# Kernel tuning notes

Hardware: AMD Instinct MI355X
Metric: run time of the kernel (lower is better)

Reference implementation:

```python
import jax, jax.numpy as jnp
import numpy as np

B, N, H, F = 256, 256, 256, 64   # batch, nodes, hidden, output
NNB = 4                          # neighbors per node (nns - 1)
HEADS = 3
S = 2 ** NNB - 1                 # nonempty subsets for Mobius Choquet
# MASK[s, i] = True iff neighbor i is in subset s (subsets 1..2^n-1)
MASK = jnp.asarray(np.array([[(s >> i) & 1 for i in range(NNB)] for s in range(1, S + 1)], dtype=bool))


def setup_inputs() -> dict:
    key = jax.random.key(0)
    ks = jax.random.split(key, 12)
    w = 0.02
    centers = jnp.arange(N, dtype=jnp.int64)[:, None]
    neigh = jax.random.randint(ks[11], (N, NNB), 0, N).astype(jnp.int64)
    local_edges = jnp.concatenate([centers, neigh], axis=1)[:, None, :]  # [N, 1, 5]
    return {
        "observation": jax.random.normal(ks[0], (B, N, H), jnp.float32),
        "action": jax.random.normal(ks[1], (B, N, H), jnp.float32),
        "V_W1": jax.random.normal(ks[2], (N, H, H), jnp.float32) * w,
        "V_b1": jnp.zeros((N, H), jnp.float32),
        "V_W2": jax.random.normal(ks[3], (N, H, F), jnp.float32) * w,
        "V_b2": jnp.zeros((N, F), jnp.float32),
        "A_W1": jax.random.normal(ks[4], (N, 2 * H, H), jnp.float32) * w,
        "A_b1": jnp.zeros((N, H), jnp.float32),
        "A_W2": jax.random.normal(ks[5], (N, H, F), jnp.float32) * w,
        "A_b2": jnp.zeros((N, F), jnp.float32),
        "chi_m": jax.random.normal(ks[6], (N, HEADS, S), jnp.float32) * w,
        "local_edges": local_edges,
    }


def _mmlp2(x, W1, b1, W2, b2):
    # per-node (multi) 2-layer MLP: first layer ReLU, second linear (act=False)
    h = jax.nn.relu(jnp.einsum('bni,nio->bno', x, W1) + b1)
    return jnp.einsum('bnh,nho->bno', h, W2) + b2


def reference(observation, action, V_W1, V_b1, V_W2, V_b2,
              A_W1, A_b1, A_W2, A_b2, chi_m, local_edges):
    V = _mmlp2(observation, V_W1, V_b1, V_W2, V_b2)                      # [B,N,F]
    A = _mmlp2(jnp.concatenate([observation, action], axis=-1),
               A_W1, A_b1, A_W2, A_b2)                                   # [B,N,F]
    Q = A + V                                                            # [B,N,F]
    centers = local_edges[:, 0, 0]        # [N]
    neigh = local_edges[:, 0, 1:]         # [N, NNB]
    # .data in torch -> detach the gathered neighbor Q-values
    Qn = jax.lax.stop_gradient(Q[:, neigh, :])                           # [B,N,NNB,F]
    # Mobius Choquet: min over each nonempty subset of neighbors
    masked = jnp.where(MASK[None, None, :, :, None], Qn[:, :, None, :, :], jnp.inf)
    mins = masked.min(axis=3)                                            # [B,N,S,F]
    chi = jnp.einsum('bnsf,nhs->bnf', mins, chi_m) / HEADS               # [B,N,F]
    return (chi + Q[:, centers, :]).mean(axis=-1)                        # [B,N]
```

## Files before the change

### kernel.cpp

```cpp
#include <hip/hip_runtime.h>
#include <cstddef>


#define BN 256
#define HD 256
#define FD 64
#define NHD (BN * HD)
#define XS 40

typedef _Float16 f16x8 __attribute__((ext_vector_type(8)));
typedef _Float16 f16x4 __attribute__((ext_vector_type(4)));
typedef float f32x4 __attribute__((ext_vector_type(4)));

#define BAR_LGKM()                                                         \
  asm volatile("s_waitcnt lgkmcnt(0)" ::: "memory");                       \
  __builtin_amdgcn_s_barrier();                                            \
  asm volatile("" ::: "memory");

__device__ __forceinline__ void x_load(const float* xs0, const float* xs1, int n,
                                       int row0, int kt, int tid, float4 xr[2]) {
  int kOff = kt * 32;
  const float* xs = (kOff < 256) ? xs0 : xs1;
  int row = tid >> 2, c = (tid & 3) * 4;
  const float* p = xs + (size_t)(row0 + row) * NHD + n * HD + (kOff & 255) + c;
  xr[0] = *(const float4*)p;
  xr[1] = *(const float4*)(p + 16);
}
__device__ __forceinline__ void x_write(_Float16* Xl, int tid, const float4 xr[2]) {
  int row = tid >> 2, c = (tid & 3) * 4;
  f16x4 a, b;
  a[0] = (_Float16)xr[0].x; a[1] = (_Float16)xr[0].y;
  a[2] = (_Float16)xr[0].z; a[3] = (_Float16)xr[0].w;
  b[0] = (_Float16)xr[1].x; b[1] = (_Float16)xr[1].y;
  b[2] = (_Float16)xr[1].z; b[3] = (_Float16)xr[1].w;
  *(f16x4*)(Xl + row * XS + c) = a;
  *(f16x4*)(Xl + row * XS + c + 16) = b;
}

__device__ __forceinline__ void w1_stage(const float* __restrict__ Wg, _Float16* Wl,
                                         int kt, int w, int l) {
#pragma unroll
  for (int cg = 0; cg < 4; ++cg) {
    int col = cg * 64 + l;
    const float* p = Wg + (size_t)(kt * 32 + w * 8) * HD + col;
    f16x8 v;
#pragma unroll
    for (int r = 0; r < 8; ++r) v[r] = (_Float16)p[(size_t)r * HD];
    *(f16x8*)(Wl + ((size_t)(w * 256 + col)) * 8) = v;
  }
}

__device__ __forceinline__ void w2_stage(const float* __restrict__ W2g, _Float16* Wl,
                                         int half, int w, int l) {
#pragma unroll
  for (int cg = 0; cg < 4; ++cg) {
    int khi = w * 4 + cg;
    const float* p = W2g + (size_t)(half * 128 + khi * 8) * FD + l;
    f16x8 v;
#pragma unroll
    for (int r = 0; r < 8; ++r) v[r] = (_Float16)p[(size_t)r * FD];
    *(f16x8*)(Wl + ((size_t)(khi * 64 + l)) * 8) = v;
  }
}

__device__ __forceinline__ void g1_compute(const _Float16* Wl, const _Float16* Xl,
                                           int lrow, int lq, int Nbase,
                                           f32x4 acc[4][4]) {
  f16x8 b[4];
#pragma unroll
  for (int nf = 0; nf < 4; ++nf)
    b[nf] = *(const f16x8*)(Wl + ((size_t)(lq * 256 + Nbase + nf * 16 + lrow)) * 8);
#pragma unroll
  for (int m = 0; m < 4; ++m) {
    f16x8 a = *(const f16x8*)(Xl + (m * 16 + lrow) * XS + lq * 8);
#pragma unroll
    for (int nf = 0; nf < 4; ++nf)
      acc[m][nf] = __builtin_amdgcn_mfma_f32_16x16x32_f16(a, b[nf], acc[m][nf], 0, 0, 0);
  }
}

template <int NK>
__device__ __forceinline__ void run_gemm1(const float* xs0, const float* xs1,
                                          const float* __restrict__ Wg,
                                          int n, int row0, int tid, int lrow, int lq,
                                          int Nbase, int w, int l,
                                          _Float16* Wl, _Float16* Xl,
                                          f32x4 acc[4][4]) {
  float4 xr[2];
  x_load(xs0, xs1, n, row0, 0, tid, xr);
  w1_stage(Wg, Wl, 0, w, l);
  x_write(Xl, tid, xr);
#pragma unroll 1
  for (int kt = 0; kt < NK; ++kt) {
    BAR_LGKM();
    if (kt + 1 < NK) x_load(xs0, xs1, n, row0, kt + 1, tid, xr);
    g1_compute(Wl, Xl, lrow, lq, Nbase, acc);
    BAR_LGKM();
    if (kt + 1 < NK) {
      w1_stage(Wg, Wl, kt + 1, w, l);
      x_write(Xl, tid, xr);
    }
  }
}

__device__ __forceinline__ void gemm2_branch(const f32x4 acc[4][4], f32x4 acc2[4],
                                             const float* __restrict__ W2g,
                                             const float* __restrict__ b1g,
                                             _Float16* Wl, _Float16* slab,
                                             int lrow, int lq, int Nbase, int w, int l) {
  float bv[4];
#pragma unroll
  for (int nf = 0; nf < 4; ++nf) bv[nf] = b1g[Nbase + nf * 16 + lrow];
  w2_stage(W2g, Wl, 0, w, l);
#pragma unroll
  for (int s = 0; s < 8; ++s) {
    if (w == (s >> 1)) {
#pragma unroll
      for (int m = 0; m < 4; ++m)
#pragma unroll
        for (int nf2 = 0; nf2 < 2; ++nf2) {
          const int nf = (s & 1) * 2 + nf2;
#pragma unroll
          for (int r = 0; r < 4; ++r)
            slab[(m * 16 + lq * 4 + r) * XS + nf2 * 16 + lrow] =
                (_Float16)fmaxf(acc[m][nf][r] + bv[nf], 0.f);
        }
    }
    BAR_LGKM();
    f16x8 a2 = *(const f16x8*)(slab + (w * 16 + lrow) * XS + lq * 8);
    f16x8 bb[4];
#pragma unroll
    for (int nf = 0; nf < 4; ++nf)
      bb[nf] = *(const f16x8*)(Wl + ((size_t)(((s & 3) * 4 + lq) * 64 + nf * 16 + lrow)) * 8);
#pragma unroll
    for (int nf = 0; nf < 4; ++nf)
      acc2[nf] = __builtin_amdgcn_mfma_f32_16x16x32_f16(a2, bb[nf], acc2[nf], 0, 0, 0);
    BAR_LGKM();
    if (s == 3) w2_stage(W2g, Wl, 1, w, l);
  }
}

__global__ __launch_bounds__(256, 4) void phase1_kernel(
    const float* __restrict__ obs, const float* __restrict__ act,
    const float* __restrict__ V_W1, const float* __restrict__ V_b1,
    const float* __restrict__ V_W2, const float* __restrict__ V_b2,
    const float* __restrict__ A_W1, const float* __restrict__ A_b1,
    const float* __restrict__ A_W2, const float* __restrict__ A_b2,
    float* __restrict__ Q) {
  __shared__ __align__(16) _Float16 Wl[8192];
  __shared__ __align__(16) _Float16 Xl[2560];

  int tid = threadIdx.x;
  int l = tid & 63, w = tid >> 6;
  int lrow = l & 15, lq = l >> 4;
  int Nbase = w * 64;
  int bid = blockIdx.x;
  int n = bid & 255;
  int row0 = (bid >> 8) * 64;

  f32x4 acc[4][4];
  f32x4 acc2[4];
#pragma unroll
  for (int j = 0; j < 4; ++j) acc2[j] = (f32x4){0.f, 0.f, 0.f, 0.f};

#pragma unroll
  for (int m = 0; m < 4; ++m)
#pragma unroll
    for (int nf = 0; nf < 4; ++nf) acc[m][nf] = (f32x4){0.f, 0.f, 0.f, 0.f};
  run_gemm1<8>(obs, obs, V_W1 + (size_t)n * HD * HD, n, row0, tid, lrow, lq,
               Nbase, w, l, Wl, Xl, acc);
  gemm2_branch(acc, acc2, V_W2 + (size_t)n * HD * FD, V_b1 + n * HD,
               Wl, Xl, lrow, lq, Nbase, w, l);

#pragma unroll
  for (int m = 0; m < 4; ++m)
#pragma unroll
    for (int nf = 0; nf < 4; ++nf) acc[m][nf] = (f32x4){0.f, 0.f, 0.f, 0.f};
  run_gemm1<16>(obs, act, A_W1 + (size_t)n * 2 * HD * HD, n, row0, tid, lrow, lq,
                Nbase, w, l, Wl, Xl, acc);
  gemm2_branch(acc, acc2, A_W2 + (size_t)n * HD * FD, A_b1 + n * HD,
               Wl, Xl, lrow, lq, Nbase, w, l);

  const float* vb2 = V_b2 + n * FD;
  const float* ab2 = A_b2 + n * FD;
#pragma unroll
  for (int nf = 0; nf < 4; ++nf) {
    int f = nf * 16 + lrow;
    float bias = vb2[f] + ab2[f];
#pragma unroll
    for (int rr = 0; rr < 4; ++rr) {
      int row = row0 + w * 16 + lq * 4 + rr;
      Q[(size_t)row * (BN * FD) + n * FD + f] = acc2[nf][rr] + bias;
    }
  }
}

__global__ __launch_bounds__(256) void phase2_kernel(const float* __restrict__ Q,
                                                     const float* __restrict__ chi_m,
                                                     const int* __restrict__ le,
                                                     float* __restrict__ out) {
  int b = blockIdx.x;
  int n = threadIdx.x;
  int step = (le[5] == 1) ? 1 : 2;
  const int* e = le + n * 5 * step;
  int c  = e[0 * step] & (BN - 1);
  int n0 = e[1 * step] & (BN - 1);
  int n1 = e[2 * step] & (BN - 1);
  int n2 = e[3 * step] & (BN - 1);
  int n3 = e[4 * step] & (BN - 1);
  const float* ch = chi_m + n * 45;
  float cm[15];
#pragma unroll
  for (int s = 0; s < 15; ++s) cm[s] = (ch[s] + ch[15 + s] + ch[30 + s]) * (1.f / 3.f);
  const float* qb = Q + (size_t)b * (BN * FD);
  const float* q0 = qb + n0 * FD;
  const float* q1 = qb + n1 * FD;
  const float* q2 = qb + n2 * FD;
  const float* q3 = qb + n3 * FD;
  const float* qc = qb + c * FD;
  float acc = 0.f;
#pragma unroll
  for (int f = 0; f < FD; f += 4) {
    float4 v0 = *(const float4*)(q0 + f);
    float4 v1 = *(const float4*)(q1 + f);
    float4 v2 = *(const float4*)(q2 + f);
    float4 v3 = *(const float4*)(q3 + f);
    float4 vc = *(const float4*)(qc + f);
    const float* p0 = (const float*)&v0;
    const float* p1 = (const float*)&v1;
    const float* p2 = (const float*)&v2;
    const float* p3 = (const float*)&v3;
    const float* pc = (const float*)&vc;
#pragma unroll
    for (int u = 0; u < 4; ++u) {
      float a = p0[u], bq = p1[u], cq = p2[u], d = p3[u];
      float m01 = fminf(a, bq), m02 = fminf(a, cq), m03 = fminf(a, d);
      float m12 = fminf(bq, cq), m13 = fminf(bq, d), m23 = fminf(cq, d);
      float m012 = fminf(m01, cq), m013 = fminf(m01, d);
      float m023 = fminf(m02, d),  m123 = fminf(m12, d);
      float m0123 = fminf(m01, m23);
      float chi = cm[0] * a   + cm[1] * bq   + cm[2] * m01  + cm[3] * cq
                + cm[4] * m02 + cm[5] * m12  + cm[6] * m012 + cm[7] * d
                + cm[8] * m03 + cm[9] * m13  + cm[10] * m013 + cm[11] * m23
                + cm[12] * m023 + cm[13] * m123 + cm[14] * m0123;
      acc += chi + pc[u];
    }
  }
  out[b * BN + n] = acc * (1.f / 64.f);
}

extern "C" void kernel_launch(void* const* d_in, const int* in_sizes, int n_in,
                              void* d_out, int out_size, void* d_ws, size_t ws_size,
                              hipStream_t stream) {
  (void)in_sizes; (void)n_in; (void)out_size; (void)ws_size;
  const float* obs  = (const float*)d_in[0];
  const float* act  = (const float*)d_in[1];
  const float* V_W1 = (const float*)d_in[2];
  const float* V_b1 = (const float*)d_in[3];
  const float* V_W2 = (const float*)d_in[4];
  const float* V_b2 = (const float*)d_in[5];
  const float* A_W1 = (const float*)d_in[6];
  const float* A_b1 = (const float*)d_in[7];
  const float* A_W2 = (const float*)d_in[8];
  const float* A_b2 = (const float*)d_in[9];
  const float* chim = (const float*)d_in[10];
  const int*   le   = (const int*)d_in[11];
  float* Q   = (float*)d_ws;
  float* out = (float*)d_out;

  phase1_kernel<<<dim3(1024), dim3(256), 0, stream>>>(obs, act, V_W1, V_b1, V_W2, V_b2,
                                                      A_W1, A_b1, A_W2, A_b2, Q);
  phase2_kernel<<<dim3(256), dim3(256), 0, stream>>>(Q, chim, le, out);
}
```

Baseline: 118.8 us.

## Prefetch W1 tiles as float4 into registers and swizzle LDS columns

The W1 staging is split into an issue step and a commit step. The next k-tile's weights are loaded as float4 vectors into registers before the MFMA compute, then converted and written to LDS after the barrier, so global latency overlaps with compute. The old per-element strided scalar loads are replaced by coalesced 16-byte loads, and an XOR swizzle on the LDS column index avoids bank conflicts from the new write pattern. This adds 32 live registers per thread, so the launch-bounds occupancy hint drops from 4 to 3 blocks per CU, which risks lower latency hiding elsewhere.

```diff
diff --git a/kernel.cpp b/kernel.cpp
--- a/kernel.cpp
+++ b/kernel.cpp
@@ -16,6 +16,8 @@
   asm volatile("s_waitcnt lgkmcnt(0)" ::: "memory");                       \
   __builtin_amdgcn_s_barrier();                                            \
   asm volatile("" ::: "memory");
+
+__device__ __forceinline__ int wswz(int col) { return col ^ ((col >> 2) & 7); }
 
 __device__ __forceinline__ void x_load(const float* xs0, const float* xs1, int n,
                                        int row0, int kt, int tid, float4 xr[2]) {
@@ -37,16 +39,26 @@
   *(f16x4*)(Xl + row * XS + c + 16) = b;
 }
 
-__device__ __forceinline__ void w1_stage(const float* __restrict__ Wg, _Float16* Wl,
-                                         int kt, int w, int l) {
-#pragma unroll
-  for (int cg = 0; cg < 4; ++cg) {
-    int col = cg * 64 + l;
-    const float* p = Wg + (size_t)(kt * 32 + w * 8) * HD + col;
+__device__ __forceinline__ void w1_issue(const float* __restrict__ Wg, int kt,
+                                         int w, int l, float4 wr[8]) {
+  const float* p = Wg + (size_t)(kt * 32 + w * 8) * HD + 4 * l;
+#pragma unroll
+  for (int r = 0; r < 8; ++r) wr[r] = *(const float4*)(p + (size_t)r * HD);
+}
+__device__ __forceinline__ void w1_commit(_Float16* Wl, int w, int l,
+                                          const float4 wr[8]) {
+#pragma unroll
+  for (int j = 0; j < 4; ++j) {
     f16x8 v;
-#pragma unroll
-    for (int r = 0; r < 8; ++r) v[r] = (_Float16)p[(size_t)r * HD];
-    *(f16x8*)(Wl + ((size_t)(w * 256 + col)) * 8) = v;
+    v[0] = (_Float16)((j == 0) ? wr[0].x : (j == 1) ? wr[0].y : (j == 2) ? wr[0].z : wr[0].w);
+    v[1] = (_Float16)((j == 0) ? wr[1].x : (j == 1) ? wr[1].y : (j == 2) ? wr[1].z : wr[1].w);
+    v[2] = (_Float16)((j == 0) ? wr[2].x : (j == 1) ? wr[2].y : (j == 2) ? wr[2].z : wr[2].w);
+    v[3] = (_Float16)((j == 0) ? wr[3].x : (j == 1) ? wr[3].y : (j == 2) ? wr[3].z : wr[3].w);
+    v[4] = (_Float16)((j == 0) ? wr[4].x : (j == 1) ? wr[4].y : (j == 2) ? wr[4].z : wr[4].w);
+    v[5] = (_Float16)((j == 0) ? wr[5].x : (j == 1) ? wr[5].y : (j == 2) ? wr[5].z : wr[5].w);
+    v[6] = (_Float16)((j == 0) ? wr[6].x : (j == 1) ? wr[6].y : (j == 2) ? wr[6].z : wr[6].w);
+    v[7] = (_Float16)((j == 0) ? wr[7].x : (j == 1) ? wr[7].y : (j == 2) ? wr[7].z : wr[7].w);
+    *(f16x8*)(Wl + (size_t)(w * 256 + wswz(4 * l + j)) * 8) = v;
   }
 }
 
@@ -64,12 +76,12 @@
 }
 
 __device__ __forceinline__ void g1_compute(const _Float16* Wl, const _Float16* Xl,
-                                           int lrow, int lq, int Nbase,
+                                           int lrow, int lq, const int wcol[4],
                                            f32x4 acc[4][4]) {
   f16x8 b[4];
 #pragma unroll
   for (int nf = 0; nf < 4; ++nf)
-    b[nf] = *(const f16x8*)(Wl + ((size_t)(lq * 256 + Nbase + nf * 16 + lrow)) * 8);
+    b[nf] = *(const f16x8*)(Wl + (size_t)(lq * 256 + wcol[nf]) * 8);
 #pragma unroll
   for (int m = 0; m < 4; ++m) {
     f16x8 a = *(const f16x8*)(Xl + (m * 16 + lrow) * XS + lq * 8);
@@ -83,21 +95,26 @@
 __device__ __forceinline__ void run_gemm1(const float* xs0, const float* xs1,
                                           const float* __restrict__ Wg,
                                           int n, int row0, int tid, int lrow, int lq,
-                                          int Nbase, int w, int l,
+                                          const int wcol[4], int w, int l,
                                           _Float16* Wl, _Float16* Xl,
                                           f32x4 acc[4][4]) {
+  float4 wr[8];
   float4 xr[2];
+  w1_issue(Wg, 0, w, l, wr);
   x_load(xs0, xs1, n, row0, 0, tid, xr);
-  w1_stage(Wg, Wl, 0, w, l);
+  w1_commit(Wl, w, l, wr);
   x_write(Xl, tid, xr);
 #pragma unroll 1
   for (int kt = 0; kt < NK; ++kt) {
     BAR_LGKM();
-    if (kt + 1 < NK) x_load(xs0, xs1, n, row0, kt + 1, tid, xr);
-    g1_compute(Wl, Xl, lrow, lq, Nbase, acc);
-    BAR_LGKM();
     if (kt + 1 < NK) {
-      w1_stage(Wg, Wl, kt + 1, w, l);
+      w1_issue(Wg, kt + 1, w, l, wr);
+      x_load(xs0, xs1, n, row0, kt + 1, tid, xr);
+    }
+    g1_compute(Wl, Xl, lrow, lq, wcol, acc);
+    BAR_LGKM();
+    if (kt + 1 < NK) {
+      w1_commit(Wl, w, l, wr);
       x_write(Xl, tid, xr);
     }
   }
@@ -140,7 +157,7 @@
   }
 }
 
-__global__ __launch_bounds__(256, 4) void phase1_kernel(
+__global__ __launch_bounds__(256, 3) void phase1_kernel(
     const float* __restrict__ obs, const float* __restrict__ act,
     const float* __restrict__ V_W1, const float* __restrict__ V_b1,
     const float* __restrict__ V_W2, const float* __restrict__ V_b2,
@@ -154,6 +171,9 @@
   int l = tid & 63, w = tid >> 6;
   int lrow = l & 15, lq = l >> 4;
   int Nbase = w * 64;
+  int wcol[4];
+#pragma unroll
+  for (int nf = 0; nf < 4; ++nf) wcol[nf] = wswz(Nbase + nf * 16 + lrow);
   int bid = blockIdx.x;
   int n = bid & 255;
   int row0 = (bid >> 8) * 64;
@@ -168,7 +188,7 @@
 #pragma unroll
     for (int nf = 0; nf < 4; ++nf) acc[m][nf] = (f32x4){0.f, 0.f, 0.f, 0.f};
   run_gemm1<8>(obs, obs, V_W1 + (size_t)n * HD * HD, n, row0, tid, lrow, lq,
-               Nbase, w, l, Wl, Xl, acc);
+               wcol, w, l, Wl, Xl, acc);
   gemm2_branch(acc, acc2, V_W2 + (size_t)n * HD * FD, V_b1 + n * HD,
                Wl, Xl, lrow, lq, Nbase, w, l);
 
@@ -177,7 +197,7 @@
 #pragma unroll
     for (int nf = 0; nf < 4; ++nf) acc[m][nf] = (f32x4){0.f, 0.f, 0.f, 0.f};
   run_gemm1<16>(obs, act, A_W1 + (size_t)n * 2 * HD * HD, n, row0, tid, lrow, lq,
-                Nbase, w, l, Wl, Xl, acc);
+                wcol, w, l, Wl, Xl, acc);
   gemm2_branch(acc, acc2, A_W2 + (size_t)n * HD * FD, A_b1 + n * HD,
                Wl, Xl, lrow, lq, Nbase, w, l);
 
```

Result: slower. 163.1 us (+37.3%).

## Stage W1 tiles via direct global-to-LDS loads in fp32 with swizzle

Applied to the files above, without the earlier changes.

Replaces the register-mediated W1 staging, which gathered and converted fp32 to fp16 per thread, with global_load_lds DMA of raw fp32 rows into a padded, XOR-swizzled LDS buffer. Conversion to fp16 now happens when the MFMA B fragments are read from LDS. The aim is to cut VGPR pressure and global-load latency exposed during staging. In exchange the LDS footprint doubles, occupancy is lowered to 3 waves per SIMD in launch bounds, each fragment needs 8 scalar LDS reads plus conversions, and the loop waits on vmcnt(0) before every barrier.

```diff
diff --git a/kernel.cpp b/kernel.cpp
--- a/kernel.cpp
+++ b/kernel.cpp
@@ -7,13 +7,23 @@
 #define FD 64
 #define NHD (BN * HD)
 #define XS 40
+#define WLS 260
 
 typedef _Float16 f16x8 __attribute__((ext_vector_type(8)));
 typedef _Float16 f16x4 __attribute__((ext_vector_type(4)));
 typedef float f32x4 __attribute__((ext_vector_type(4)));
 
+#define GLOAD16(g, l)                                              \
+  __builtin_amdgcn_global_load_lds(                                \
+      (__attribute__((address_space(1))) void*)(g),                \
+      (__attribute__((address_space(3))) void*)(l), 16, 0, 0)
+
 #define BAR_LGKM()                                                         \
   asm volatile("s_waitcnt lgkmcnt(0)" ::: "memory");                       \
+  __builtin_amdgcn_s_barrier();                                            \
+  asm volatile("" ::: "memory");
+#define VMCNT0_BAR()                                                       \
+  asm volatile("s_waitcnt vmcnt(0) lgkmcnt(0)" ::: "memory");              \
   __builtin_amdgcn_s_barrier();                                            \
   asm volatile("" ::: "memory");
 
@@ -37,16 +47,13 @@
   *(f16x4*)(Xl + row * XS + c + 16) = b;
 }
 
-__device__ __forceinline__ void w1_stage(const float* __restrict__ Wg, _Float16* Wl,
-                                         int kt, int w, int l) {
-#pragma unroll
-  for (int cg = 0; cg < 4; ++cg) {
-    int col = cg * 64 + l;
-    const float* p = Wg + (size_t)(kt * 32 + w * 8) * HD + col;
-    f16x8 v;
-#pragma unroll
-    for (int r = 0; r < 8; ++r) v[r] = (_Float16)p[(size_t)r * HD];
-    *(f16x8*)(Wl + ((size_t)(w * 256 + col)) * 8) = v;
+__device__ __forceinline__ void w_gload(const float* __restrict__ Wg, float* Wl,
+                                        int kt, int w, int l) {
+  int xoff = (l ^ ((w & 1) << 2)) << 2;
+#pragma unroll
+  for (int s = 0; s < 8; ++s) {
+    int row = w * 8 + s;
+    GLOAD16(Wg + (size_t)(kt * 32 + row) * HD + xoff, Wl + (size_t)row * WLS);
   }
 }
 
@@ -63,13 +70,19 @@
   }
 }
 
-__device__ __forceinline__ void g1_compute(const _Float16* Wl, const _Float16* Xl,
-                                           int lrow, int lq, int Nbase,
+__device__ __forceinline__ void g1_compute(const float* Wl, const _Float16* Xl,
+                                           int lrow, int lq, const int wcol[4],
                                            f32x4 acc[4][4]) {
+  const float* wbase = Wl + (size_t)(lq * 8) * WLS;
   f16x8 b[4];
 #pragma unroll
-  for (int nf = 0; nf < 4; ++nf)
-    b[nf] = *(const f16x8*)(Wl + ((size_t)(lq * 256 + Nbase + nf * 16 + lrow)) * 8);
+  for (int nf = 0; nf < 4; ++nf) {
+    const float* p = wbase + wcol[nf];
+    f16x8 t;
+#pragma unroll
+    for (int j = 0; j < 8; ++j) t[j] = (_Float16)p[(size_t)j * WLS];
+    b[nf] = t;
+  }
 #pragma unroll
   for (int m = 0; m < 4; ++m) {
     f16x8 a = *(const f16x8*)(Xl + (m * 16 + lrow) * XS + lq * 8);
@@ -83,24 +96,26 @@
 __device__ __forceinline__ void run_gemm1(const float* xs0, const float* xs1,
                                           const float* __restrict__ Wg,
                                           int n, int row0, int tid, int lrow, int lq,
-                                          int Nbase, int w, int l,
-                                          _Float16* Wl, _Float16* Xl,
+                                          const int wcol[4], int w, int l,
+                                          float* Wl, _Float16* Xl,
                                           f32x4 acc[4][4]) {
   float4 xr[2];
   x_load(xs0, xs1, n, row0, 0, tid, xr);
-  w1_stage(Wg, Wl, 0, w, l);
+  w_gload(Wg, Wl, 0, w, l);
   x_write(Xl, tid, xr);
+  VMCNT0_BAR();
 #pragma unroll 1
   for (int kt = 0; kt < NK; ++kt) {
-    BAR_LGKM();
     if (kt + 1 < NK) x_load(xs0, xs1, n, row0, kt + 1, tid, xr);
-    g1_compute(Wl, Xl, lrow, lq, Nbase, acc);
+    g1_compute(Wl, Xl, lrow, lq, wcol, acc);
     BAR_LGKM();
     if (kt + 1 < NK) {
-      w1_stage(Wg, Wl, kt + 1, w, l);
+      w_gload(Wg, Wl, kt + 1, w, l);
       x_write(Xl, tid, xr);
-    }
-  }
+      VMCNT0_BAR();
+    }
+  }
+  BAR_LGKM();
 }
 
 __device__ __forceinline__ void gemm2_branch(const f32x4 acc[4][4], f32x4 acc2[4],
@@ -140,20 +155,24 @@
   }
 }
 
-__global__ __launch_bounds__(256, 4) void phase1_kernel(
+__global__ __launch_bounds__(256, 3) void phase1_kernel(
     const float* __restrict__ obs, const float* __restrict__ act,
     const float* __restrict__ V_W1, const float* __restrict__ V_b1,
     const float* __restrict__ V_W2, const float* __restrict__ V_b2,
     const float* __restrict__ A_W1, const float* __restrict__ A_b1,
     const float* __restrict__ A_W2, const float* __restrict__ A_b2,
     float* __restrict__ Q) {
-  __shared__ __align__(16) _Float16 Wl[8192];
+  __shared__ __align__(16) float Wbuf[32 * WLS];
   __shared__ __align__(16) _Float16 Xl[2560];
 
   int tid = threadIdx.x;
   int l = tid & 63, w = tid >> 6;
   int lrow = l & 15, lq = l >> 4;
   int Nbase = w * 64;
+  int wcol[4];
+#pragma unroll
+  for (int nf = 0; nf < 4; ++nf)
+    wcol[nf] = (Nbase + nf * 16 + lrow) ^ ((lq & 1) << 4);
   int bid = blockIdx.x;
   int n = bid & 255;
   int row0 = (bid >> 8) * 64;
@@ -168,18 +187,18 @@
 #pragma unroll
     for (int nf = 0; nf < 4; ++nf) acc[m][nf] = (f32x4){0.f, 0.f, 0.f, 0.f};
   run_gemm1<8>(obs, obs, V_W1 + (size_t)n * HD * HD, n, row0, tid, lrow, lq,
-               Nbase, w, l, Wl, Xl, acc);
+               wcol, w, l, Wbuf, Xl, acc);
   gemm2_branch(acc, acc2, V_W2 + (size_t)n * HD * FD, V_b1 + n * HD,
-               Wl, Xl, lrow, lq, Nbase, w, l);
+               (_Float16*)Wbuf, Xl, lrow, lq, Nbase, w, l);
 
 #pragma unroll
   for (int m = 0; m < 4; ++m)
 #pragma unroll
     for (int nf = 0; nf < 4; ++nf) acc[m][nf] = (f32x4){0.f, 0.f, 0.f, 0.f};
   run_gemm1<16>(obs, act, A_W1 + (size_t)n * 2 * HD * HD, n, row0, tid, lrow, lq,
-                Nbase, w, l, Wl, Xl, acc);
+                wcol, w, l, Wbuf, Xl, acc);
   gemm2_branch(acc, acc2, A_W2 + (size_t)n * HD * FD, A_b1 + n * HD,
-               Wl, Xl, lrow, lq, Nbase, w, l);
+               (_Float16*)Wbuf, Xl, lrow, lq, Nbase, w, l);
 
   const float* vb2 = V_b2 + n * FD;
   const float* ab2 = A_b2 + n * FD;
```

Measured after the change: 186.3 us. +56.9%, slower.

## Load W1 fragments directly into registers with two-stage prefetch, drop LDS staging

Applied to the files above, without the earlier changes.

The first-layer GEMM no longer stages W1 through shared memory. Each lane loads its own B fragments from global memory into registers, double-buffered two k-tiles ahead, and packs them to fp16 right before the MFMA. The block-index mapping is reordered so blocks that share a node's weights run close together, and launch bounds drop to 2 blocks per CU to make room for the larger register footprint. This cuts LDS traffic and barrier stalls on weights, at the cost of more registers, lower occupancy and scattered uncoalesced global loads.

```diff
diff --git a/kernel.cpp b/kernel.cpp
--- a/kernel.cpp
+++ b/kernel.cpp
@@ -16,6 +16,13 @@
   asm volatile("s_waitcnt lgkmcnt(0)" ::: "memory");                       \
   __builtin_amdgcn_s_barrier();                                            \
   asm volatile("" ::: "memory");
+
+__device__ __forceinline__ f16x8 pack8(const float v[8]) {
+  f16x8 r;
+#pragma unroll
+  for (int i = 0; i < 8; ++i) r[i] = (_Float16)v[i];
+  return r;
+}
 
 __device__ __forceinline__ void x_load(const float* xs0, const float* xs1, int n,
                                        int row0, int kt, int tid, float4 xr[2]) {
@@ -37,17 +44,55 @@
   *(f16x4*)(Xl + row * XS + c + 16) = b;
 }
 
-__device__ __forceinline__ void w1_stage(const float* __restrict__ Wg, _Float16* Wl,
-                                         int kt, int w, int l) {
-#pragma unroll
-  for (int cg = 0; cg < 4; ++cg) {
-    int col = cg * 64 + l;
-    const float* p = Wg + (size_t)(kt * 32 + w * 8) * HD + col;
-    f16x8 v;
-#pragma unroll
-    for (int r = 0; r < 8; ++r) v[r] = (_Float16)p[(size_t)r * HD];
-    *(f16x8*)(Wl + ((size_t)(w * 256 + col)) * 8) = v;
-  }
+__device__ __forceinline__ void w1_load(const float* __restrict__ wb, float wf[4][8]) {
+#pragma unroll
+  for (int nf = 0; nf < 4; ++nf)
+#pragma unroll
+    for (int j = 0; j < 8; ++j) wf[nf][j] = wb[(size_t)j * HD + nf * 16];
+}
+
+__device__ __forceinline__ void g1_compute(const f16x8 b[4], const _Float16* Xl,
+                                           int lrow, int lq, f32x4 acc[4][4]) {
+#pragma unroll
+  for (int m = 0; m < 4; ++m) {
+    f16x8 a = *(const f16x8*)(Xl + (m * 16 + lrow) * XS + lq * 8);
+#pragma unroll
+    for (int nf = 0; nf < 4; ++nf)
+      acc[m][nf] = __builtin_amdgcn_mfma_f32_16x16x32_f16(a, b[nf], acc[m][nf], 0, 0, 0);
+  }
+}
+
+#define G1_STEP(KT, WFC)                                                     \
+  {                                                                          \
+    const int kt_ = (KT);                                                    \
+    BAR_LGKM()                             \
+    f16x8 bfr[4];                      \
+    _Pragma("unroll") for (int nf = 0; nf < 4; ++nf) bfr[nf] = pack8(WFC[nf]); \
+    if (kt_ + 2 < NK) w1_load(wb + (size_t)(kt_ + 2) * 32 * HD, WFC);        \
+    if (kt_ + 1 < NK) x_load(xs0, xs1, n, row0, kt_ + 1, tid, xr);           \
+    g1_compute(bfr, Xl, lrow, lq, acc);                                      \
+    BAR_LGKM()                             \
+    if (kt_ + 1 < NK) x_write(Xl, tid, xr);         \
+  }
+
+template <int NK>
+__device__ __forceinline__ void run_gemm1(const float* xs0, const float* xs1,
+                                          const float* __restrict__ Wg,
+                                          int n, int row0, int tid, int lrow, int lq,
+                                          int Nbase, _Float16* Xl, f32x4 acc[4][4]) {
+  const float* wb = Wg + (size_t)(lq * 8) * HD + Nbase + lrow;
+  float wfA[4][8], wfB[4][8];
+  float4 xr[2];
+  w1_load(wb, wfA);
+  w1_load(wb + (size_t)32 * HD, wfB);
+  x_load(xs0, xs1, n, row0, 0, tid, xr);
+  x_write(Xl, tid, xr);
+#pragma unroll 1
+  for (int kt = 0; kt < NK; kt += 2) {
+    G1_STEP(kt, wfA)
+    G1_STEP(kt + 1, wfB)
+  }
+  BAR_LGKM()
 }
 
 __device__ __forceinline__ void w2_stage(const float* __restrict__ W2g, _Float16* Wl,
@@ -60,46 +105,6 @@
 #pragma unroll
     for (int r = 0; r < 8; ++r) v[r] = (_Float16)p[(size_t)r * FD];
     *(f16x8*)(Wl + ((size_t)(khi * 64 + l)) * 8) = v;
-  }
-}
-
-__device__ __forceinline__ void g1_compute(const _Float16* Wl, const _Float16* Xl,
-                                           int lrow, int lq, int Nbase,
-                                           f32x4 acc[4][4]) {
-  f16x8 b[4];
-#pragma unroll
-  for (int nf = 0; nf < 4; ++nf)
-    b[nf] = *(const f16x8*)(Wl + ((size_t)(lq * 256 + Nbase + nf * 16 + lrow)) * 8);
-#pragma unroll
-  for (int m = 0; m < 4; ++m) {
-    f16x8 a = *(const f16x8*)(Xl + (m * 16 + lrow) * XS + lq * 8);
-#pragma unroll
-    for (int nf = 0; nf < 4; ++nf)
-      acc[m][nf] = __builtin_amdgcn_mfma_f32_16x16x32_f16(a, b[nf], acc[m][nf], 0, 0, 0);
-  }
-}
-
-template <int NK>
-__device__ __forceinline__ void run_gemm1(const float* xs0, const float* xs1,
-                                          const float* __restrict__ Wg,
-                                          int n, int row0, int tid, int lrow, int lq,
-                                          int Nbase, int w, int l,
-                                          _Float16* Wl, _Float16* Xl,
-                                          f32x4 acc[4][4]) {
-  float4 xr[2];
-  x_load(xs0, xs1, n, row0, 0, tid, xr);
-  w1_stage(Wg, Wl, 0, w, l);
-  x_write(Xl, tid, xr);
-#pragma unroll 1
-  for (int kt = 0; kt < NK; ++kt) {
-    BAR_LGKM();
-    if (kt + 1 < NK) x_load(xs0, xs1, n, row0, kt + 1, tid, xr);
-    g1_compute(Wl, Xl, lrow, lq, Nbase, acc);
-    BAR_LGKM();
-    if (kt + 1 < NK) {
-      w1_stage(Wg, Wl, kt + 1, w, l);
-      x_write(Xl, tid, xr);
-    }
   }
 }
 
@@ -140,7 +145,7 @@
   }
 }
 
-__global__ __launch_bounds__(256, 4) void phase1_kernel(
+__global__ __launch_bounds__(256, 2) void phase1_kernel(
     const float* __restrict__ obs, const float* __restrict__ act,
     const float* __restrict__ V_W1, const float* __restrict__ V_b1,
     const float* __restrict__ V_W2, const float* __restrict__ V_b2,
@@ -155,8 +160,8 @@
   int lrow = l & 15, lq = l >> 4;
   int Nbase = w * 64;
   int bid = blockIdx.x;
-  int n = bid & 255;
-  int row0 = (bid >> 8) * 64;
+  int n = ((bid >> 5) << 3) | (bid & 7);
+  int row0 = ((bid >> 3) & 3) * 64;
 
   f32x4 acc[4][4];
   f32x4 acc2[4];
@@ -167,8 +172,12 @@
   for (int m = 0; m < 4; ++m)
 #pragma unroll
     for (int nf = 0; nf < 4; ++nf) acc[m][nf] = (f32x4){0.f, 0.f, 0.f, 0.f};
-  run_gemm1<8>(obs, obs, V_W1 + (size_t)n * HD * HD, n, row0, tid, lrow, lq,
-               Nbase, w, l, Wl, Xl, acc);
+  {
+    const int NK = 8;
+    const float* xs0 = obs; const float* xs1 = obs;
+    const float* Wg = V_W1 + (size_t)n * HD * HD;
+    run_gemm1<8>(xs0, xs1, Wg, n, row0, tid, lrow, lq, Nbase, Xl, acc);
+  }
   gemm2_branch(acc, acc2, V_W2 + (size_t)n * HD * FD, V_b1 + n * HD,
                Wl, Xl, lrow, lq, Nbase, w, l);
 
@@ -176,8 +185,11 @@
   for (int m = 0; m < 4; ++m)
 #pragma unroll
     for (int nf = 0; nf < 4; ++nf) acc[m][nf] = (f32x4){0.f, 0.f, 0.f, 0.f};
-  run_gemm1<16>(obs, act, A_W1 + (size_t)n * 2 * HD * HD, n, row0, tid, lrow, lq,
-                Nbase, w, l, Wl, Xl, acc);
+  {
+    const float* xs0 = obs; const float* xs1 = act;
+    const float* Wg = A_W1 + (size_t)n * 2 * HD * HD;
+    run_gemm1<16>(xs0, xs1, Wg, n, row0, tid, lrow, lq, Nbase, Xl, acc);
+  }
   gemm2_branch(acc, acc2, A_W2 + (size_t)n * HD * FD, A_b1 + n * HD,
                Wl, Xl, lrow, lq, Nbase, w, l);
 
```

After: 126.8 us. +6.8%, slower.
